# Kernel tuning notes

Measured on AMD Instinct MI355X. Metric: run time of the kernel, lower is better.

The kernel has to match this reference:

```python
import jax, jax.numpy as jnp
import numpy as np

B, C, H, W = 16, 256, 48, 160
BASELINE = 0.54
REL_ELEV = 1.65
H_MEAN = 1.535


def setup_inputs() -> dict:
    key = jax.random.key(0)
    k = jax.random.split(key, 5)
    features = jax.random.normal(k[0], (B, C, H, W), dtype=jnp.float32)
    # realistic KITTI-style P2 (full-resolution intrinsics; forward divides rows 0:2 by 16)
    base = np.zeros((3, 4), np.float32)
    base[0, 0] = 721.5; base[1, 1] = 721.5
    base[0, 2] = 609.5; base[1, 2] = 172.8
    base[2, 2] = 1.0;   base[1, 3] = 0.2
    P2 = jnp.asarray(base)[None] + 0.5 * jax.random.uniform(k[1], (B, 3, 4), dtype=jnp.float32)
    w_disp = 0.05 * jax.random.normal(k[2], (1, C, 3, 3), dtype=jnp.float32)  # disp_create conv3x3
    b_disp = jnp.zeros((1,), jnp.float32)
    w_ext = 0.05 * jax.random.normal(k[3], (C, C + 1), dtype=jnp.float32)     # extract conv1x1 (O,I)
    b_ext = jnp.zeros((C,), jnp.float32)
    alpha = 0.5 * jnp.ones((1,), jnp.float32)  # nn.Parameter (init 0.0; nonzero to exercise path)
    return {"features": features, "P2": P2, "w_disp": w_disp, "b_disp": b_disp,
            "w_ext": w_ext, "b_ext": b_ext, "alpha": alpha}


def _grid_sample_border(feat, gx, gy):
    """Bilinear grid_sample, padding_mode='border', align_corners=True.
    feat: (B,C1,H,W); gx, gy: (B,H,W) in [-1,1]."""
    Bs, C1, Hs, Ws = feat.shape
    ix = jnp.clip((gx + 1.0) * 0.5 * (Ws - 1), 0.0, Ws - 1)
    iy = jnp.clip((gy + 1.0) * 0.5 * (Hs - 1), 0.0, Hs - 1)
    ix0 = jnp.floor(ix); iy0 = jnp.floor(iy)
    ix1 = jnp.minimum(ix0 + 1.0, Ws - 1); iy1 = jnp.minimum(iy0 + 1.0, Hs - 1)
    wx = (ix - ix0).reshape(Bs, 1, -1)
    wy = (iy - iy0).reshape(Bs, 1, -1)
    flat = feat.reshape(Bs, C1, Hs * Ws)

    def gather(f, yq, xq):
        idx = (yq * Ws + xq).astype(jnp.int32).reshape(-1)
        return f[:, idx]  # (C1, H*W)

    g = jax.vmap(gather)
    v00 = g(flat, iy0, ix0); v01 = g(flat, iy0, ix1)
    v10 = g(flat, iy1, ix0); v11 = g(flat, iy1, ix1)
    out = (v00 * (1 - wx) * (1 - wy) + v01 * wx * (1 - wy)
           + v10 * (1 - wx) * wy + v11 * wx * wy)
    return out.reshape(Bs, C1, Hs, Ws)


def reference(features, P2, w_disp, b_disp, w_ext, b_ext, alpha):
    x = features
    Bs = x.shape[0]
    P2 = P2.at[:, 0:2].set(P2[:, 0:2] / 16.0)
    # disp_create: conv3x3 -> tanh, then detach-scaled
    d = jax.lax.conv_general_dilated(x, w_disp, (1, 1), 'SAME',
                                     dimension_numbers=('NCHW', 'OIHW', 'NCHW'))
    d = jnp.tanh(d + b_disp[None, :, None, None])
    disp = 0.1 * (0.05 * d + 0.95 * jax.lax.stop_gradient(d))  # (B,1,H,W)

    yy = jnp.arange(H, dtype=jnp.float32)[None, :, None]  # (1,H,1): row index
    fy = P2[:, 1:2, 1:2]; cy = P2[:, 1:2, 2:3]; Ty = P2[:, 1:2, 3:4]  # (B,1,1)
    disparity = jax.nn.relu(fy * BASELINE * (yy - cy)
                            / (jnp.abs(fy * REL_ELEV + Ty) + 1e-10))  # (B,H,1)
    disparity = jnp.broadcast_to(disparity, (Bs, H, W))

    x_base = jnp.broadcast_to(jnp.linspace(-1.0, 1.0, W, dtype=jnp.float32)[None, None, :], (Bs, H, W))
    y_base = jnp.linspace(-1.0, 1.0, H, dtype=jnp.float32)[None, :, None]  # (1,H,1)
    y_shifts_base = jax.nn.relu(H_MEAN * (yy - cy) / (2.0 * (REL_ELEV - 0.5 * H_MEAN))) / (H * 0.5)
    y_shifts = y_shifts_base + disp[:, 0]  # (B,H,W)
    gy = y_base + y_shifts

    feats = jnp.concatenate([disparity[:, None], x], axis=1)  # (B,C+1,H,W)
    samp = _grid_sample_border(feats, x_base, gy)
    out = jnp.einsum('oc,bchw->bohw', w_ext, samp) + b_ext[None, :, None, None]
    return jax.nn.relu(x + out * alpha[0])
```

## Files before the change

### kernel.cpp

```cpp
#include <hip/hip_runtime.h>
#include <stdint.h>

#define NB 16
#define NC 256
#define NH 48
#define NW 160
#define HW (NH*NW)
#define NP (NB*HW)

static __device__ __forceinline__ unsigned short f2bf(float f){
  union { float f; uint32_t u; } v; v.f = f;
  uint32_t u = v.u;
  uint32_t r = (u + 0x7FFFu + ((u >> 16) & 1u)) >> 16;
  return (unsigned short)r;
}
static __device__ __forceinline__ float bf2f(unsigned short h){
  union { float f; uint32_t u; } v; v.u = ((uint32_t)h) << 16; return v.f;
}

__global__ __launch_bounds__(256) void kw_conv(const float* __restrict__ w_ext,
                                               const float* __restrict__ w_disp,
                                               unsigned short* __restrict__ WbF,
                                               unsigned short* __restrict__ WtapF){
  int d = blockIdx.x * 256 + threadIdx.x;
  if (blockIdx.x < 256){
    int j  = d & 7;
    int lane = (d >> 3) & 63;
    int mi = (d >> 9) & 3;
    int w  = (d >> 11) & 3;
    int ks = d >> 13;
    int m = w * 64 + mi * 16 + (lane & 15);
    int k = ks * 32 + (lane >> 4) * 8 + j;
    WbF[d] = f2bf(w_ext[m * 257 + 1 + k]);
  } else {
    int d2 = d - 65536;
    int j  = d2 & 7;
    int lane = (d2 >> 3) & 63;
    int ks = d2 >> 9;
    int tap = lane & 15;
    int k = ks * 32 + (lane >> 4) * 8 + j;
    WtapF[d2] = (tap < 9) ? f2bf(w_disp[k * 9 + tap]) : (unsigned short)0;
  }
}

typedef __attribute__((ext_vector_type(8))) short bf16x8;
typedef __attribute__((ext_vector_type(4))) float f32x4;

__global__ __launch_bounds__(256) void kb_gemm(
    const float* __restrict__ x,
    const unsigned short* __restrict__ Wb,
    const unsigned short* __restrict__ Wtap,
    unsigned short* __restrict__ U,
    float* __restrict__ T)
{
  __shared__ __align__(16) unsigned short smem[2][4 * 512];
  int bx = blockIdx.x;
  int b  = bx / 120;
  int nt = bx - b * 120;
  int p0 = nt * 64;

  int tid  = threadIdx.x;
  int lane = tid & 63;
  int w    = tid >> 6;
  int l15 = lane & 15;
  int lq  = lane >> 4;

  int sn  = tid & 63;
  int skq = tid >> 6;
  const float* xbase = x + ((size_t)b * NC) * HW + p0 + sn;
  const int swroff = (sn >> 4) * 512 + ((sn & 15) + skq * 16) * 8;

  f32x4 zero = {0.f, 0.f, 0.f, 0.f};
  f32x4 acc[4][4];
  f32x4 acct[4];
  #pragma unroll
  for (int mi = 0; mi < 4; ++mi){
    acct[mi] = zero;
    #pragma unroll
    for (int ni = 0; ni < 4; ++ni) acc[mi][ni] = zero;
  }

  float r0[8], r1[8];
  bf16x8 afA[4], afB[4];
  bf16x8 atA = {0,0,0,0,0,0,0,0}, atB = {0,0,0,0,0,0,0,0};
  #pragma unroll
  for (int j = 0; j < 8; ++j) r0[j] = xbase[(size_t)(skq * 8 + j) * HW];
  #pragma unroll
  for (int j = 0; j < 8; ++j) r1[j] = xbase[(size_t)(32 + skq * 8 + j) * HW];
  #pragma unroll
  for (int mi = 0; mi < 4; ++mi)
    afA[mi] = *(const bf16x8*)(Wb + ((0 * 16 + w * 4 + mi) << 9) + lane * 8);
  if (w == 0)
    atA = *(const bf16x8*)(Wtap + (0 << 9) + lane * 8);
  {
    unsigned short h[8];
    #pragma unroll
    for (int j = 0; j < 8; ++j) h[j] = f2bf(r0[j]);
    *(bf16x8*)(smem[0] + swroff) = *(bf16x8*)h;
  }
  asm volatile("s_waitcnt lgkmcnt(0)" ::: "memory");
  __builtin_amdgcn_sched_barrier(0);
  __builtin_amdgcn_s_barrier();
  __builtin_amdgcn_sched_barrier(0);

#define KB_ITER(T_, RCUR, RNXT, AFC, AFN, ATC, ATN)                           \
  {                                                                           \
    constexpr int t_ = (T_);                                                  \
    if (t_ + 2 < 8) {                                                         \
      _Pragma("unroll")                                                       \
      for (int j = 0; j < 8; ++j)                                             \
        RCUR[j] = xbase[(size_t)((t_ + 2) * 32 + skq * 8 + j) * HW];          \
    }                                                                         \
    if (t_ + 1 < 8) {                                                         \
      _Pragma("unroll")                                                       \
      for (int mi = 0; mi < 4; ++mi)                                          \
        AFN[mi] = *(const bf16x8*)(Wb + (((t_ + 1) * 16 + w * 4 + mi) << 9)   \
                                   + lane * 8);                               \
      if (w == 0)                                                             \
        ATN = *(const bf16x8*)(Wtap + ((t_ + 1) << 9) + lane * 8);            \
    }                                                                         \
    bf16x8 bg[4];                                                             \
    _Pragma("unroll")                                                         \
    for (int ni = 0; ni < 4; ++ni)                                            \
      bg[ni] = *(const bf16x8*)(smem[t_ & 1] + ni * 512 + lane * 8);          \
    _Pragma("unroll")                                                         \
    for (int mi = 0; mi < 4; ++mi)                                            \
      _Pragma("unroll")                                                       \
      for (int ni = 0; ni < 4; ++ni)                                          \
        acc[mi][ni] = __builtin_amdgcn_mfma_f32_16x16x32_bf16(AFC[mi], bg[ni],\
                                                      acc[mi][ni], 0, 0, 0);  \
    if (w == 0) {                                                             \
      _Pragma("unroll")                                                       \
      for (int ni = 0; ni < 4; ++ni)                                          \
        acct[ni] = __builtin_amdgcn_mfma_f32_16x16x32_bf16(ATC, bg[ni],       \
                                                       acct[ni], 0, 0, 0);    \
    }                                                                         \
    if (t_ + 1 < 8) {                                                         \
      unsigned short h[8];                                                    \
      _Pragma("unroll")                                                       \
      for (int j = 0; j < 8; ++j) h[j] = f2bf(RNXT[j]);                       \
      *(bf16x8*)(smem[(t_ + 1) & 1] + swroff) = *(bf16x8*)h;                  \
      asm volatile("s_waitcnt lgkmcnt(0)" ::: "memory");                      \
      __builtin_amdgcn_sched_barrier(0);                                      \
      __builtin_amdgcn_s_barrier();                                           \
      __builtin_amdgcn_sched_barrier(0);                                      \
    }                                                                         \
  }

  KB_ITER(0, r0, r1, afA, afB, atA, atB)
  KB_ITER(1, r1, r0, afB, afA, atB, atA)
  KB_ITER(2, r0, r1, afA, afB, atA, atB)
  KB_ITER(3, r1, r0, afB, afA, atB, atA)
  KB_ITER(4, r0, r1, afA, afB, atA, atB)
  KB_ITER(5, r1, r0, afB, afA, atB, atA)
  KB_ITER(6, r0, r1, afA, afB, atA, atB)
  KB_ITER(7, r1, r0, afB, afA, atB, atA)
#undef KB_ITER

  #pragma unroll
  for (int mi = 0; mi < 4; ++mi){
    #pragma unroll
    for (int ni = 0; ni < 4; ++ni){
      int o = w * 64 + mi * 16 + lq * 4;
      int n = ni * 16 + l15;
      size_t base = ((size_t)(b * NC + o)) * HW + p0 + n;
      #pragma unroll
      for (int r = 0; r < 4; ++r)
        U[base + (size_t)r * HW] = f2bf(acc[mi][ni][r]);
    }
  }
  if (w == 0){
    #pragma unroll
    for (int ni = 0; ni < 4; ++ni){
      int n = ni * 16 + l15;
      #pragma unroll
      for (int r = 0; r < 4; ++r){
        int k = lq * 4 + r;
        if (k < 9)
          T[(size_t)k * NP + (size_t)b * HW + p0 + n] = acct[ni][r];
      }
    }
  }
}

__global__ __launch_bounds__(256) void kp_grid(
    const float* __restrict__ P2, const float* __restrict__ b_disp,
    const float* __restrict__ T, float4* __restrict__ pre)
{
  int p = blockIdx.x * 256 + threadIdx.x;
  int b  = p / HW;
  int hw = p - b * HW;
  int y  = hw / NW;
  int xx = hw - y * NW;

  float d = 0.f;
  #pragma unroll
  for (int ky = 0; ky < 3; ++ky){
    int yy2 = y + ky - 1;
    if (yy2 < 0 || yy2 >= NH) continue;
    #pragma unroll
    for (int kx = 0; kx < 3; ++kx){
      int xx2 = xx + kx - 1;
      if (xx2 < 0 || xx2 >= NW) continue;
      d += T[(size_t)(ky * 3 + kx) * NP + b * HW + yy2 * NW + xx2];
    }
  }
  float th = tanhf(d + b_disp[0]);

  float fy = P2[b * 12 + 5] * 0.0625f;
  float cy = P2[b * 12 + 6] * 0.0625f;
  float Ty = P2[b * 12 + 7] * 0.0625f;

  float ysb   = fmaxf(1.535f * ((float)y - cy) / 1.765f, 0.f) * (1.f / 24.f);
  float ybase = -1.f + (float)y * (2.f / 47.f);
  float gy = ybase + ysb + 0.1f * th;
  float iy = fminf(fmaxf((gy + 1.f) * 0.5f * 47.f, 0.f), 47.f);
  float fiy0 = floorf(iy);
  float wy = iy - fiy0;
  int iy0 = (int)fiy0;
  int iy1 = min(iy0 + 1, 47);

  float inv_den = 1.f / (fabsf(fy * 1.65f + Ty) + 1e-10f);
  float dr0 = fmaxf(fy * 0.54f * ((float)iy0 - cy) * inv_den, 0.f);
  float dr1 = fmaxf(fy * 0.54f * ((float)iy1 - cy) * inv_den, 0.f);
  float dlerp = (1.f - wy) * dr0 + wy * dr1;

  float4 pr;
  pr.x = wy; pr.y = dlerp;
  pr.z = __int_as_float(iy0 * NW + xx);
  pr.w = __int_as_float(iy1 * NW + xx);
  pre[p] = pr;
}

__global__ __launch_bounds__(256) void kc_epilogue(
    const float* __restrict__ x, const float* __restrict__ w_ext,
    const float* __restrict__ b_ext, const float* __restrict__ alpha,
    const unsigned short* __restrict__ U, const float4* __restrict__ pre,
    float* __restrict__ out)
{
  int bx = blockIdx.x;
  int ptile = bx >> 3;
  int cg    = bx & 7;
  int p = ptile * 256 + threadIdx.x;
  int b  = p / HW;
  int hw = p - b * HW;

  float4 pr = pre[p];
  float wy    = pr.x;
  float dlerp = pr.y;
  int off0 = __float_as_int(pr.z);
  int off1 = __float_as_int(pr.w);
  float w1 = 1.f - wy;
  float al = alpha[0];

  size_t base0 = (size_t)(b * NC) * HW;
  const unsigned short* Ub = U + base0;
  const float* xb = x + base0 + hw;
  float* ob = out + base0 + hw;

  int o0 = cg * 32;
  #pragma unroll 4
  for (int o = o0; o < o0 + 32; ++o){
    float u0 = bf2f(Ub[(size_t)o * HW + off0]);
    float u1 = bf2f(Ub[(size_t)o * HW + off1]);
    float val = w1 * u0 + wy * u1 + w_ext[o * 257] * dlerp + b_ext[o];
    float r = xb[(size_t)o * HW] + al * val;
    ob[(size_t)o * HW] = fmaxf(r, 0.f);
  }
}

extern "C" void kernel_launch(void* const* d_in, const int* in_sizes, int n_in,
                              void* d_out, int out_size, void* d_ws, size_t ws_size,
                              hipStream_t stream) {
  const float* features = (const float*)d_in[0];
  const float* P2       = (const float*)d_in[1];
  const float* w_disp   = (const float*)d_in[2];
  const float* b_disp   = (const float*)d_in[3];
  const float* w_ext    = (const float*)d_in[4];
  const float* b_ext    = (const float*)d_in[5];
  const float* alpha    = (const float*)d_in[6];
  float* out = (float*)d_out;

  char* ws = (char*)d_ws;
  const size_t U_bytes   = (size_t)NP * 256 * 2;
  const size_t T_bytes   = (size_t)9 * NP * 4;
  const size_t pre_bytes = (size_t)NP * 16;
  unsigned short* U    = (unsigned short*)ws;
  float*          T    = (float*)(ws + U_bytes);
  float4*         pre  = (float4*)(ws + U_bytes + T_bytes);
  unsigned short* Wb   = (unsigned short*)(ws + U_bytes + T_bytes + pre_bytes);
  unsigned short* Wtap = Wb + 256 * 256;

  hipLaunchKernelGGL(kw_conv,     dim3(272),  dim3(256), 0, stream, w_ext, w_disp, Wb, Wtap);
  hipLaunchKernelGGL(kb_gemm,     dim3(1920), dim3(256), 0, stream, features, Wb, Wtap, U, T);
  hipLaunchKernelGGL(kp_grid,     dim3(480),  dim3(256), 0, stream, P2, b_disp, T, pre);
  hipLaunchKernelGGL(kc_epilogue, dim3(3840), dim3(256), 0, stream,
                     features, w_ext, b_ext, alpha, U, pre, out);
}
```

Before: 305.8 us.

## Stage full K-slab of x into LDS upfront and drop per-step barriers

```diff
diff --git a/kernel.cpp b/kernel.cpp
--- a/kernel.cpp
+++ b/kernel.cpp
@@ -46,14 +46,14 @@
 typedef __attribute__((ext_vector_type(8))) short bf16x8;
 typedef __attribute__((ext_vector_type(4))) float f32x4;
 
-__global__ __launch_bounds__(256) void kb_gemm(
+__global__ __launch_bounds__(256, 3) void kb_gemm(
     const float* __restrict__ x,
     const unsigned short* __restrict__ Wb,
     const unsigned short* __restrict__ Wtap,
     unsigned short* __restrict__ U,
     float* __restrict__ T)
 {
-  __shared__ __align__(16) unsigned short smem[2][4 * 512];
+  __shared__ __align__(16) unsigned short smem[8 * 2048];
   int bx = blockIdx.x;
   int b  = bx / 120;
   int nt = bx - b * 120;
@@ -68,7 +68,15 @@
   int sn  = tid & 63;
   int skq = tid >> 6;
   const float* xbase = x + ((size_t)b * NC) * HW + p0 + sn;
-  const int swroff = (sn >> 4) * 512 + ((sn & 15) + skq * 16) * 8;
+  unsigned short* swr = smem + (sn >> 4) * 512 + ((sn & 15) + skq * 16) * 8;
+
+  bf16x8 afA[4], afB[4];
+  bf16x8 atA = {0,0,0,0,0,0,0,0}, atB = {0,0,0,0,0,0,0,0};
+  #pragma unroll
+  for (int mi = 0; mi < 4; ++mi)
+    afA[mi] = *(const bf16x8*)(Wb + ((w * 4 + mi) << 9) + lane * 8);
+  if (w == 0)
+    atA = *(const bf16x8*)(Wtap + lane * 8);
 
   f32x4 zero = {0.f, 0.f, 0.f, 0.f};
   f32x4 acc[4][4];
@@ -80,37 +88,33 @@
     for (int ni = 0; ni < 4; ++ni) acc[mi][ni] = zero;
   }
 
-  float r0[8], r1[8];
-  bf16x8 afA[4], afB[4];
-  bf16x8 atA = {0,0,0,0,0,0,0,0}, atB = {0,0,0,0,0,0,0,0};
-  #pragma unroll
-  for (int j = 0; j < 8; ++j) r0[j] = xbase[(size_t)(skq * 8 + j) * HW];
-  #pragma unroll
-  for (int j = 0; j < 8; ++j) r1[j] = xbase[(size_t)(32 + skq * 8 + j) * HW];
-  #pragma unroll
-  for (int mi = 0; mi < 4; ++mi)
-    afA[mi] = *(const bf16x8*)(Wb + ((0 * 16 + w * 4 + mi) << 9) + lane * 8);
-  if (w == 0)
-    atA = *(const bf16x8*)(Wtap + (0 << 9) + lane * 8);
-  {
-    unsigned short h[8];
-    #pragma unroll
-    for (int j = 0; j < 8; ++j) h[j] = f2bf(r0[j]);
-    *(bf16x8*)(smem[0] + swroff) = *(bf16x8*)h;
-  }
-  asm volatile("s_waitcnt lgkmcnt(0)" ::: "memory");
-  __builtin_amdgcn_sched_barrier(0);
-  __builtin_amdgcn_s_barrier();
-  __builtin_amdgcn_sched_barrier(0);
-
-#define KB_ITER(T_, RCUR, RNXT, AFC, AFN, ATC, ATN)                           \
+  float rA[8], rB[8];
+#define LOADX(R, KS)                                                          \
+  { _Pragma("unroll")                                                         \
+    for (int j = 0; j < 8; ++j)                                               \
+      R[j] = xbase[(size_t)((KS) * 32 + skq * 8 + j) * HW]; }
+#define CVW(R, KS)                                                            \
+  { unsigned short h[8];                                                      \
+    _Pragma("unroll")                                                         \
+    for (int j = 0; j < 8; ++j) h[j] = f2bf(R[j]);                            \
+    *(bf16x8*)(swr + (KS) * 2048) = *(bf16x8*)h; }
+
+  LOADX(rA, 0) LOADX(rB, 1)
+  CVW(rA, 0)   LOADX(rA, 2)
+  CVW(rB, 1)   LOADX(rB, 3)
+  CVW(rA, 2)   LOADX(rA, 4)
+  CVW(rB, 3)   LOADX(rB, 5)
+  CVW(rA, 4)   LOADX(rA, 6)
+  CVW(rB, 5)   LOADX(rB, 7)
+  CVW(rA, 6)
+  CVW(rB, 7)
+#undef LOADX
+#undef CVW
+  __syncthreads();
+
+#define KB_STEP(T_, AFC, AFN, ATC, ATN)                                       \
   {                                                                           \
     constexpr int t_ = (T_);                                                  \
-    if (t_ + 2 < 8) {                                                         \
-      _Pragma("unroll")                                                       \
-      for (int j = 0; j < 8; ++j)                                             \
-        RCUR[j] = xbase[(size_t)((t_ + 2) * 32 + skq * 8 + j) * HW];          \
-    }                                                                         \
     if (t_ + 1 < 8) {                                                         \
       _Pragma("unroll")                                                       \
       for (int mi = 0; mi < 4; ++mi)                                          \
@@ -122,7 +126,7 @@
     bf16x8 bg[4];                                                             \
     _Pragma("unroll")                                                         \
     for (int ni = 0; ni < 4; ++ni)                                            \
-      bg[ni] = *(const bf16x8*)(smem[t_ & 1] + ni * 512 + lane * 8);          \
+      bg[ni] = *(const bf16x8*)(smem + t_ * 2048 + ni * 512 + lane * 8);      \
     _Pragma("unroll")                                                         \
     for (int mi = 0; mi < 4; ++mi)                                            \
       _Pragma("unroll")                                                       \
@@ -135,27 +139,17 @@
         acct[ni] = __builtin_amdgcn_mfma_f32_16x16x32_bf16(ATC, bg[ni],       \
                                                        acct[ni], 0, 0, 0);    \
     }                                                                         \
-    if (t_ + 1 < 8) {                                                         \
-      unsigned short h[8];                                                    \
-      _Pragma("unroll")                                                       \
-      for (int j = 0; j < 8; ++j) h[j] = f2bf(RNXT[j]);                       \
-      *(bf16x8*)(smem[(t_ + 1) & 1] + swroff) = *(bf16x8*)h;                  \
-      asm volatile("s_waitcnt lgkmcnt(0)" ::: "memory");                      \
-      __builtin_amdgcn_sched_barrier(0);                                      \
-      __builtin_amdgcn_s_barrier();                                           \
-      __builtin_amdgcn_sched_barrier(0);                                      \
-    }                                                                         \
-  }
-
-  KB_ITER(0, r0, r1, afA, afB, atA, atB)
-  KB_ITER(1, r1, r0, afB, afA, atB, atA)
-  KB_ITER(2, r0, r1, afA, afB, atA, atB)
-  KB_ITER(3, r1, r0, afB, afA, atB, atA)
-  KB_ITER(4, r0, r1, afA, afB, atA, atB)
-  KB_ITER(5, r1, r0, afB, afA, atB, atA)
-  KB_ITER(6, r0, r1, afA, afB, atA, atB)
-  KB_ITER(7, r1, r0, afB, afA, atB, atA)
-#undef KB_ITER
+  }
+
+  KB_STEP(0, afA, afB, atA, atB)
+  KB_STEP(1, afB, afA, atB, atA)
+  KB_STEP(2, afA, afB, atA, atB)
+  KB_STEP(3, afB, afA, atB, atA)
+  KB_STEP(4, afA, afB, atA, atB)
+  KB_STEP(5, afB, afA, atB, atA)
+  KB_STEP(6, afA, afB, atA, atB)
+  KB_STEP(7, afB, afA, atB, atA)
+#undef KB_STEP
 
   #pragma unroll
   for (int mi = 0; mi < 4; ++mi){
```

Result: no change. 308.0 us (+0.7%).
